# Kernel optimization log

Measured on AMD Instinct MI355X. Metric: run time of the kernel, lower is better.

Reference implementation:

```python
import jax, jax.numpy as jnp
import numpy as np

B, LQ, LM = 8, 128, 512
Q_SIZE, M_SIZE, H_SIZE = 512, 512, 256
MASKED_VALUE = -1e24


def setup_inputs() -> dict:
    key = jax.random.key(0)
    ks = jax.random.split(key, 8)
    query = jax.random.normal(ks[0], (B, LQ, Q_SIZE), dtype=jnp.float32)
    memory = jax.random.normal(ks[1], (B, LM, M_SIZE), dtype=jnp.float32)
    mask = jax.random.randint(ks[2], (B, LM), 0, 2).astype(bool)
    s_q = 1.0 / np.sqrt(Q_SIZE)
    s_m = 1.0 / np.sqrt(M_SIZE)
    s_h = 1.0 / np.sqrt(H_SIZE)
    Wq = jax.random.uniform(ks[3], (Q_SIZE, H_SIZE), jnp.float32, -s_q, s_q)
    bq = jax.random.uniform(ks[4], (H_SIZE,), jnp.float32, -s_q, s_q)
    Wm = jax.random.uniform(ks[5], (M_SIZE, H_SIZE), jnp.float32, -s_m, s_m)
    v = jax.random.uniform(ks[6], (H_SIZE,), jnp.float32, -s_h, s_h)
    return {"query": query, "memory": memory, "mask": mask,
            "Wq": Wq, "bq": bq, "Wm": Wm, "v": v}


def reference(query, memory, mask, Wq, bq, Wm, v):
    # mlp (Bahdanau) attention; key defaults to memory
    q_proj = jnp.einsum('bqd,dh->bqh', query, Wq) + bq      # [B,Lq,H]
    k_proj = jnp.einsum('bmd,dh->bmh', memory, Wm)          # [B,Lm,H]
    hidden = jnp.tanh(q_proj[:, :, None, :] + k_proj[:, None, :, :])  # [B,Lq,Lm,H]
    attn = jnp.einsum('bqmh,h->bqm', hidden, v)             # [B,Lq,Lm]
    attn = jnp.where(mask[:, None, :], MASKED_VALUE, attn)
    weights = jax.nn.softmax(attn, axis=-1)
    weighted_memory = jnp.einsum('bqm,bmd->bqd', weights, memory)
    return weighted_memory, weights
```

## Files before the change

kernel.cpp:

```cpp
#include <hip/hip_runtime.h>
#include <hip/hip_bf16.h>

#define B_   8
#define LQ_  128
#define LM_  512
#define D_   512
#define H_   256
#define MASKVAL -1e24f
#define PRESCALE 2.88539008177792681f

typedef __attribute__((ext_vector_type(8))) short bf16x8;
typedef __attribute__((ext_vector_type(4))) float f32x4;

__device__ __forceinline__ ushort f2bf(float x) {
    return __builtin_bit_cast(ushort, __float2bfloat16(x));
}

#define PBM 32
#define PBN 32
#define PBK 64
#define PLDK 88

__global__ __launch_bounds__(256) void proj_mfma(
    const float* __restrict__ query, const float* __restrict__ memory,
    const float* __restrict__ Wq, const float* __restrict__ Wm,
    const float* __restrict__ bq,
    float* __restrict__ qp, float* __restrict__ kT4)
{
    __shared__ ushort As[PBM][PLDK];
    __shared__ ushort Bs[PBN][PLDK];
    __shared__ float  T[PBM][33];

    const int mtile = blockIdx.x % 160;
    const int ntile = blockIdx.x / 160;
    const int n0 = ntile * PBN;
    const bool is_q = (mtile < 32);
    const float* X = is_q ? (query  + (size_t)mtile * PBM * D_)
                          : (memory + (size_t)(mtile - 32) * PBM * D_);
    const float* W = is_q ? Wq : Wm;

    const int t = threadIdx.x;
    const int lane = t & 63, w = t >> 6;
    const int wm = (w & 1) * 16, wn = (w >> 1) * 16;
    const int ar  = t >> 4;
    const int akq = t & 15;
    const int frow = lane & 15;
    const int fkof = (lane >> 4) * 8;

    f32x4 acc = {0.f, 0.f, 0.f, 0.f};

    for (int k0 = 0; k0 < D_; k0 += PBK) {
#pragma unroll
        for (int p = 0; p < 2; ++p) {
            const int row = ar + p * 16;
            const float4 x4 = *(const float4*)(X + (size_t)row * D_ + k0 + akq * 4);
            ushort4 u4;
            u4.x = f2bf(x4.x); u4.y = f2bf(x4.y); u4.z = f2bf(x4.z); u4.w = f2bf(x4.w);
            *(ushort4*)&As[row][akq * 4] = u4;
        }
#pragma unroll
        for (int p = 0; p < 2; ++p) {
            const int L  = t + p * 256;
            const int kk = L >> 3;
            const int f4 = L & 7;
            const float4 w4 = *(const float4*)(W + (size_t)(k0 + kk) * H_ + n0 + f4 * 4);
            Bs[f4 * 4 + 0][kk] = f2bf(w4.x);
            Bs[f4 * 4 + 1][kk] = f2bf(w4.y);
            Bs[f4 * 4 + 2][kk] = f2bf(w4.z);
            Bs[f4 * 4 + 3][kk] = f2bf(w4.w);
        }
        __syncthreads();
#pragma unroll
        for (int ks = 0; ks < PBK; ks += 32) {
            bf16x8 a = *(const bf16x8*)&As[wm + frow][ks + fkof];
            bf16x8 b = *(const bf16x8*)&Bs[wn + frow][ks + fkof];
            acc = __builtin_amdgcn_mfma_f32_16x16x32_bf16(a, b, acc, 0, 0, 0);
        }
        __syncthreads();
    }

    const int lane16 = lane & 15;
    const int rloc = wm + (lane >> 4) * 4;
    if (is_q) {
        const int col = n0 + wn + lane16;
        const float bias = bq[col];
        float* out = qp + (size_t)mtile * PBM * H_;
#pragma unroll
        for (int r = 0; r < 4; ++r)
            out[(size_t)(rloc + r) * H_ + col] =
                __builtin_amdgcn_exp2f((acc[r] + bias) * PRESCALE);
    } else {
#pragma unroll
        for (int r = 0; r < 4; ++r)
            T[rloc + r][wn + lane16] = __builtin_amdgcn_exp2f(acc[r] * PRESCALE);
        __syncthreads();
        const int m_local = t & 31;
        const int hq = t >> 5;
        const int h0 = hq * 4;
        float4 o;
        o.x = T[m_local][h0 + 0];
        o.y = T[m_local][h0 + 1];
        o.z = T[m_local][h0 + 2];
        o.w = T[m_local][h0 + 3];
        float* dst = kT4 + ((size_t)(n0 / 4 + hq) * 4096 + (size_t)(mtile - 32) * 32 + m_local) * 4;
        *(float4*)dst = o;
    }
}

__global__ __launch_bounds__(512, 4) void score_softmax(
    const float* __restrict__ qp,
    const float* __restrict__ kT4,
    const int*   __restrict__ mask,
    const float* __restrict__ v,
    float* __restrict__ out_w,
    ushort* __restrict__ wbf)
{
    __shared__ float scores[2][512];

    const int t = threadIdx.x;
    const int b  = blockIdx.x & 7;
    const int qg = blockIdx.x >> 3;
    const int rowbase = b * LQ_ + qg * 2;
    const int w = t >> 6, lane = t & 63;

    {
        const int m = t;
        const float* kbase = kT4 + ((size_t)b * 512 + m) * 4;
        const float* q0r = qp + (size_t)(rowbase + 0) * 256;
        const float* q1r = qp + (size_t)(rowbase + 1) * 256;
        float acc0 = 0.f, acc1 = 0.f;
#define QUAD(ACC, SQ, K, SV) { \
        const float u_ = fmaf(SQ.x, K.x, 1.f); \
        const float w_ = fmaf(SQ.y, K.y, 1.f); \
        const float y_ = fmaf(SQ.z, K.z, 1.f); \
        const float z_ = fmaf(SQ.w, K.w, 1.f); \
        const float d12_ = u_ * w_, d34_ = y_ * z_; \
        const float n12_ = fmaf(SV.y, u_, SV.x * w_); \
        const float n34_ = fmaf(SV.w, y_, SV.z * z_); \
        const float N_ = fmaf(n12_, d34_, n34_ * d12_); \
        ACC = fmaf(N_, __builtin_amdgcn_rcpf(d12_ * d34_), ACC); }
#pragma unroll 4
        for (int h4 = 0; h4 < 64; ++h4) {
            const float4 k4 = *(const float4*)(kbase + (size_t)h4 * 16384);
            const float4 sv = *(const float4*)(v   + h4 * 4);
            const float4 s0 = *(const float4*)(q0r + h4 * 4);
            const float4 s1 = *(const float4*)(q1r + h4 * 4);
            QUAD(acc0, s0, k4, sv)
            QUAD(acc1, s1, k4, sv)
        }
#undef QUAD
        scores[0][m] = -2.f * acc0;
        scores[1][m] = -2.f * acc1;
    }
    __syncthreads();

    if (w < 2) {
        const int q = w, row = rowbase + q;
        float s[8], e[8];
        float mx = -INFINITY;
#pragma unroll
        for (int k = 0; k < 8; ++k) {
            const int m = lane + 64 * k;
            s[k] = mask[b * 512 + m] ? MASKVAL : scores[q][m];
            mx = fmaxf(mx, s[k]);
        }
#pragma unroll
        for (int off = 32; off >= 1; off >>= 1) mx = fmaxf(mx, __shfl_xor(mx, off));
        float sum = 0.0f;
#pragma unroll
        for (int k = 0; k < 8; ++k) {
            e[k] = __builtin_amdgcn_exp2f((s[k] - mx) * 1.44269504088896341f);
            sum += e[k];
        }
#pragma unroll
        for (int off = 32; off >= 1; off >>= 1) sum += __shfl_xor(sum, off);
        const float rs = __builtin_amdgcn_rcpf(sum);
#pragma unroll
        for (int k = 0; k < 8; ++k) {
            const int m = lane + 64 * k;
            const float wt = e[k] * rs;
            out_w[(size_t)row * 512 + m] = wt;
            wbf[(size_t)row * 512 + m] = f2bf(wt);
        }
    }
}

__global__ __launch_bounds__(256) void pv_mfma(
    const ushort* __restrict__ wbf,
    const float* __restrict__ memory,
    float* __restrict__ out_wm)
{
    __shared__ ushort As[PBM][PLDK];
    __shared__ ushort Bs[PBN][PLDK];

    const int b    = blockIdx.x & 7;
    const int rest = blockIdx.x >> 3;
    const int mt   = rest & 3;
    const int nt   = rest >> 2;
    const int n0   = nt * PBN;
    const ushort* A = wbf + ((size_t)b * LQ_ + mt * PBM) * 512;
    const float*  Bm = memory + (size_t)b * 512 * 512;

    const int t = threadIdx.x;
    const int lane = t & 63, w = t >> 6;
    const int wm = (w & 1) * 16, wn = (w >> 1) * 16;
    const int ar  = t >> 4;
    const int akq = t & 15;
    const int frow = lane & 15;
    const int fkof = (lane >> 4) * 8;

    f32x4 acc = {0.f, 0.f, 0.f, 0.f};

    for (int k0 = 0; k0 < 512; k0 += PBK) {
#pragma unroll
        for (int p = 0; p < 2; ++p) {
            const int row = ar + p * 16;
            *(ushort4*)&As[row][akq * 4] =
                *(const ushort4*)(A + (size_t)row * 512 + k0 + akq * 4);
        }
#pragma unroll
        for (int p = 0; p < 2; ++p) {
            const int L  = t + p * 256;
            const int kk = L >> 3;
            const int f4 = L & 7;
            const float4 w4 = *(const float4*)(Bm + (size_t)(k0 + kk) * 512 + n0 + f4 * 4);
            Bs[f4 * 4 + 0][kk] = f2bf(w4.x);
            Bs[f4 * 4 + 1][kk] = f2bf(w4.y);
            Bs[f4 * 4 + 2][kk] = f2bf(w4.z);
            Bs[f4 * 4 + 3][kk] = f2bf(w4.w);
        }
        __syncthreads();
#pragma unroll
        for (int ks = 0; ks < PBK; ks += 32) {
            bf16x8 a = *(const bf16x8*)&As[wm + frow][ks + fkof];
            bf16x8 b2 = *(const bf16x8*)&Bs[wn + frow][ks + fkof];
            acc = __builtin_amdgcn_mfma_f32_16x16x32_bf16(a, b2, acc, 0, 0, 0);
        }
        __syncthreads();
    }

    const int col  = n0 + wn + (lane & 15);
    const int rloc = wm + (lane >> 4) * 4;
    float* out = out_wm + ((size_t)b * LQ_ + mt * PBM) * 512;
#pragma unroll
    for (int r = 0; r < 4; ++r)
        out[(size_t)(rloc + r) * 512 + col] = acc[r];
}

extern "C" void kernel_launch(void* const* d_in, const int* in_sizes, int n_in,
                              void* d_out, int out_size, void* d_ws, size_t ws_size,
                              hipStream_t stream) {
    const float* query  = (const float*)d_in[0];
    const float* memory = (const float*)d_in[1];
    const int*   mask   = (const int*)  d_in[2];
    const float* Wq     = (const float*)d_in[3];
    const float* bq     = (const float*)d_in[4];
    const float* Wm     = (const float*)d_in[5];
    const float* v      = (const float*)d_in[6];

    float* out_wm = (float*)d_out;
    float* out_w  = out_wm + (size_t)B_ * LQ_ * D_;

    float*  qp  = (float*)d_ws;
    float*  kT4 = qp + (size_t)B_ * LQ_ * H_;
    ushort* wbf = (ushort*)(kT4 + (size_t)64 * 4096 * 4);

    hipLaunchKernelGGL(proj_mfma, dim3(160 * (H_ / PBN)), dim3(256), 0, stream,
                       query, memory, Wq, Wm, bq, qp, kT4);
    hipLaunchKernelGGL(score_softmax, dim3(B_ * (LQ_ / 2)), dim3(512), 0, stream,
                       qp, kT4, mask, v, out_w, wbf);
    hipLaunchKernelGGL(pv_mfma, dim3(8 * 64), dim3(256), 0, stream,
                       wbf, memory, out_wm);
}
```

Measured before the change: 40.69 us.

## Pre-transpose memory to bf16 and drop LDS staging in PV GEMM

Adds a separate kernel that transposes each batch's memory matrix to a d-major bf16 layout in workspace. The PV kernel then loads MFMA fragments straight from global memory with no shared-memory staging and no __syncthreads, removing the per-block fp32-to-bf16 conversion and scattered LDS stores. The cost is an extra kernel launch plus a full read of memory and a 4 MB bf16 write. The PV fragment loads are now 16-byte strided global reads with no reuse across the block.

```diff
diff --git a/kernel.cpp b/kernel.cpp
--- a/kernel.cpp
+++ b/kernel.cpp
@@ -105,6 +105,33 @@
         float* dst = kT4 + ((size_t)(n0 / 4 + hq) * 4096 + (size_t)(mtile - 32) * 32 + m_local) * 4;
         *(float4*)dst = o;
     }
+}
+
+__global__ __launch_bounds__(256) void memT_kernel(
+    const float* __restrict__ memory,
+    ushort* __restrict__ memTT)
+{
+    __shared__ float T[32][36];
+    const int b    = blockIdx.x & 7;
+    const int rest = blockIdx.x >> 3;
+    const int mt   = rest & 15;
+    const int dt   = rest >> 4;
+    const int t = threadIdx.x;
+
+    const int mr = t >> 3;
+    const int dc = (t & 7) * 4;
+    const float4 x4 = *(const float4*)(memory + ((size_t)b * 512 + mt * 32 + mr) * 512 + dt * 32 + dc);
+    *(float4*)&T[mr][dc] = x4;
+    __syncthreads();
+
+    const int dr = t >> 3;
+    const int mc = (t & 7) * 4;
+    ushort4 u4;
+    u4.x = f2bf(T[mc + 0][dr]);
+    u4.y = f2bf(T[mc + 1][dr]);
+    u4.z = f2bf(T[mc + 2][dr]);
+    u4.w = f2bf(T[mc + 3][dr]);
+    *(ushort4*)&memTT[((size_t)b * 512 + dt * 32 + dr) * 512 + mt * 32 + mc] = u4;
 }
 
 __global__ __launch_bounds__(512, 4) void score_softmax(
@@ -187,64 +214,38 @@
 
 __global__ __launch_bounds__(256) void pv_mfma(
     const ushort* __restrict__ wbf,
-    const float* __restrict__ memory,
+    const ushort* __restrict__ memTT,
     float* __restrict__ out_wm)
 {
-    __shared__ ushort As[PBM][PLDK];
-    __shared__ ushort Bs[PBN][PLDK];
-
     const int b    = blockIdx.x & 7;
     const int rest = blockIdx.x >> 3;
     const int mt   = rest & 3;
     const int nt   = rest >> 2;
+    const int rowA = b * LQ_ + mt * PBM;
     const int n0   = nt * PBN;
-    const ushort* A = wbf + ((size_t)b * LQ_ + mt * PBM) * 512;
-    const float*  Bm = memory + (size_t)b * 512 * 512;
 
     const int t = threadIdx.x;
     const int lane = t & 63, w = t >> 6;
     const int wm = (w & 1) * 16, wn = (w >> 1) * 16;
-    const int ar  = t >> 4;
-    const int akq = t & 15;
     const int frow = lane & 15;
     const int fkof = (lane >> 4) * 8;
 
+    const ushort* arow = wbf   + (size_t)(rowA + wm + frow) * 512 + fkof;
+    const ushort* brow = memTT + ((size_t)b * 512 + n0 + wn + frow) * 512 + fkof;
+
     f32x4 acc = {0.f, 0.f, 0.f, 0.f};
-
-    for (int k0 = 0; k0 < 512; k0 += PBK) {
-#pragma unroll
-        for (int p = 0; p < 2; ++p) {
-            const int row = ar + p * 16;
-            *(ushort4*)&As[row][akq * 4] =
-                *(const ushort4*)(A + (size_t)row * 512 + k0 + akq * 4);
-        }
-#pragma unroll
-        for (int p = 0; p < 2; ++p) {
-            const int L  = t + p * 256;
-            const int kk = L >> 3;
-            const int f4 = L & 7;
-            const float4 w4 = *(const float4*)(Bm + (size_t)(k0 + kk) * 512 + n0 + f4 * 4);
-            Bs[f4 * 4 + 0][kk] = f2bf(w4.x);
-            Bs[f4 * 4 + 1][kk] = f2bf(w4.y);
-            Bs[f4 * 4 + 2][kk] = f2bf(w4.z);
-            Bs[f4 * 4 + 3][kk] = f2bf(w4.w);
-        }
-        __syncthreads();
-#pragma unroll
-        for (int ks = 0; ks < PBK; ks += 32) {
-            bf16x8 a = *(const bf16x8*)&As[wm + frow][ks + fkof];
-            bf16x8 b2 = *(const bf16x8*)&Bs[wn + frow][ks + fkof];
-            acc = __builtin_amdgcn_mfma_f32_16x16x32_bf16(a, b2, acc, 0, 0, 0);
-        }
-        __syncthreads();
+#pragma unroll
+    for (int k0 = 0; k0 < 512; k0 += 32) {
+        bf16x8 a  = *(const bf16x8*)(arow + k0);
+        bf16x8 bb = *(const bf16x8*)(brow + k0);
+        acc = __builtin_amdgcn_mfma_f32_16x16x32_bf16(a, bb, acc, 0, 0, 0);
     }
 
     const int col  = n0 + wn + (lane & 15);
     const int rloc = wm + (lane >> 4) * 4;
-    float* out = out_wm + ((size_t)b * LQ_ + mt * PBM) * 512;
 #pragma unroll
     for (int r = 0; r < 4; ++r)
-        out[(size_t)(rloc + r) * 512 + col] = acc[r];
+        out_wm[(size_t)(rowA + rloc + r) * 512 + col] = acc[r];
 }
 
 extern "C" void kernel_launch(void* const* d_in, const int* in_sizes, int n_in,
@@ -261,14 +262,17 @@
     float* out_wm = (float*)d_out;
     float* out_w  = out_wm + (size_t)B_ * LQ_ * D_;
 
-    float*  qp  = (float*)d_ws;
-    float*  kT4 = qp + (size_t)B_ * LQ_ * H_;
-    ushort* wbf = (ushort*)(kT4 + (size_t)64 * 4096 * 4);
+    float*  qp    = (float*)d_ws;
+    float*  kT4   = qp + (size_t)B_ * LQ_ * H_;
+    ushort* wbf   = (ushort*)(kT4 + (size_t)64 * 4096 * 4);
+    ushort* memTT = wbf + (size_t)B_ * LQ_ * LM_;
 
     hipLaunchKernelGGL(proj_mfma, dim3(160 * (H_ / PBN)), dim3(256), 0, stream,
                        query, memory, Wq, Wm, bq, qp, kT4);
+    hipLaunchKernelGGL(memT_kernel, dim3(8 * 256), dim3(256), 0, stream,
+                       memory, memTT);
     hipLaunchKernelGGL(score_softmax, dim3(B_ * (LQ_ / 2)), dim3(512), 0, stream,
                        qp, kT4, mask, v, out_w, wbf);
     hipLaunchKernelGGL(pv_mfma, dim3(8 * 64), dim3(256), 0, stream,
-                       wbf, memory, out_wm);
-}
+                       wbf, memTT, out_wm);
+}
```

Result: slower. 45.91 us (+12.8%).
